# Performance work log

Hardware: AMD Instinct MI355X
Metric: run time of the kernel (lower is better)

## Reference

```python
import jax, jax.numpy as jnp
import numpy as np
from jax import lax

B, CIN, COUT, H, W = 16, 64, 64, 128, 128

def _conv(x, w, b):
    # NCHW conv, 3x3, stride 1, SAME padding (matches nn.Conv2d(k=3,s=1,p=1))
    y = lax.conv_general_dilated(x, w, (1, 1), 'SAME',
                                 dimension_numbers=('NCHW', 'OIHW', 'NCHW'))
    return y + b[None, :, None, None]

def setup_inputs() -> dict:
    key = jax.random.key(0)
    k1, k2, k3, k4, k5 = jax.random.split(key, 5)
    x = jax.random.normal(k1, (B, CIN, H, W), dtype=jnp.float32)
    w_pre = jax.random.normal(k2, (COUT * 4, CIN, 3, 3), dtype=jnp.float32) * 0.05
    b_pre = jax.random.normal(k3, (COUT * 4,), dtype=jnp.float32) * 0.05
    w_post = jax.random.normal(k4, (COUT, COUT, 3, 3), dtype=jnp.float32) * 0.05
    b_post = jax.random.normal(k5, (COUT,), dtype=jnp.float32) * 0.05
    return {'x': x, 'w_pre': w_pre, 'b_pre': b_pre, 'w_post': w_post, 'b_post': b_post}

def reference(x, w_pre, b_pre, w_post, b_post):
    t = _conv(x, w_pre, b_pre)                      # [B, 4C, H, W]
    C = t.shape[1] // 4
    ll = t[:, :C]
    lh = t[:, C:2 * C]      # passed as cV ('ad') to pywt.idwt2
    hl = t[:, 2 * C:3 * C]  # passed as cH ('da')
    hh = t[:, 3 * C:]       # cD ('dd')
    # original detaches coeffs before pywt.idwt2 (grad cut); replicate exactly
    ll, lh, hl, hh = (lax.stop_gradient(v) for v in (ll, lh, hl, hh))
    # orthonormal Haar inverse DWT (pywt 'haar' convention):
    ee = 0.5 * (ll + lh + hl + hh)  # x[2i,   2j]
    eo = 0.5 * (ll - lh + hl - hh)  # x[2i,   2j+1]
    oe = 0.5 * (ll + lh - hl - hh)  # x[2i+1, 2j]
    oo = 0.5 * (ll - lh - hl + hh)  # x[2i+1, 2j+1]
    b, c, h, w = ll.shape
    up = jnp.stack([ee, eo, oe, oo], axis=-1).reshape(b, c, h, w, 2, 2)
    up = up.transpose(0, 1, 2, 4, 3, 5).reshape(b, c, 2 * h, 2 * w)  # pixel shuffle
    return _conv(up, w_post, b_post)
```

## Files before the change

### kernel.cpp

```cpp
#include <hip/hip_runtime.h>
#include <hip/hip_bf16.h>

typedef __attribute__((ext_vector_type(8))) short bf16x8;
typedef __attribute__((ext_vector_type(4))) float f32x4;
typedef __attribute__((ext_vector_type(4))) int   i32x4;

static __device__ __forceinline__ short f2bf(float f) {
  __hip_bfloat16 h = __float2bfloat16(f);
  return *reinterpret_cast<short*>(&h);
}

__global__ __launch_bounds__(256) void prep_xb_k(const float* __restrict__ x,
                                                 short* __restrict__ xb) {
  int u = blockIdx.x * 256 + threadIdx.x;
  int c8  = u & 7;
  int pxl = u >> 3;
  int b   = pxl >> 14;
  int yx  = pxl & 16383;
  bf16x8 r;
  #pragma unroll
  for (int j = 0; j < 8; ++j)
    r[j] = f2bf(x[(b * 64 + c8 * 8 + j) * 16384 + yx]);
  *reinterpret_cast<bf16x8*>(xb + pxl * 64 + c8 * 8) = r;
}

__global__ __launch_bounds__(256) void prep_w1_k(const float* __restrict__ w,
                                                 short* __restrict__ wb) {
  int u = blockIdx.x * 256 + threadIdx.x;
  int o = u / 576;
  int k = u - o * 576;
  int tap = k >> 6, ci = k & 63;
  wb[u] = f2bf(w[(o * 64 + ci) * 9 + tap]);
}

__global__ __launch_bounds__(256) void prep_w2_k(const float* __restrict__ w,
                                                 short* __restrict__ wb) {
  int u = blockIdx.x * 256 + threadIdx.x;
  int o = u / 576;
  int k = u - o * 576;
  int tap = k >> 6, ci = k & 63;
  wb[u] = f2bf(w[(o * 64 + ci) * 9 + tap]);
}

__global__ __launch_bounds__(256) void conv1_k(
    const short* __restrict__ xb,
    const short* __restrict__ wb1,
    const float* __restrict__ b_pre,
    short* __restrict__ up)
{
  __shared__ __align__(16) char sm[25344];
  const int tid = threadIdx.x;
  const int x0  = (blockIdx.x & 1) << 6;
  const int y   = blockIdx.y;
  const int b   = blockIdx.z;

  for (int u = tid; u < 1584; u += 256) {
    int row = u / 528;
    int rem = u - row * 528;
    int px  = rem >> 3;
    int g   = rem & 7;
    int gy  = y + row - 1;
    int gx  = x0 - 1 + px;
    i32x4 v = {0, 0, 0, 0};
    if ((unsigned)gy < 128u && (unsigned)gx < 128u)
      v = *reinterpret_cast<const i32x4*>(xb + (((b << 7) + gy) << 7) * 64 + gx * 64 + g * 8);
    *reinterpret_cast<i32x4*>(sm + ((row * 66 + px) << 7) + ((g * 16) ^ ((px & 7) << 4))) = v;
  }
  __syncthreads();

  const int lane = tid & 63;
  const int wid  = tid >> 6;
  const int ln15 = lane & 15;
  const int g4   = lane >> 4;
  const int cw   = wid << 4;

  f32x4 acc[4][4];
  #pragma unroll
  for (int m = 0; m < 4; ++m)
    #pragma unroll
    for (int v = 0; v < 4; ++v)
      acc[m][v] = (f32x4){0.f, 0.f, 0.f, 0.f};

  for (int tap = 0; tap < 9; ++tap) {
    const int kh = tap / 3;
    const int kw = tap - kh * 3;
    bf16x8 bf[2][4];
    #pragma unroll
    for (int ks = 0; ks < 2; ++ks)
      #pragma unroll
      for (int v = 0; v < 4; ++v)
        bf[ks][v] = *reinterpret_cast<const bf16x8*>(
            wb1 + (v * 64 + cw + ln15) * 576 + tap * 64 + ks * 32 + g4 * 8);
    #pragma unroll
    for (int ks = 0; ks < 2; ++ks) {
      bf16x8 af[4];
      #pragma unroll
      for (int m = 0; m < 4; ++m) {
        int px = m * 16 + ln15 + kw;
        af[m] = *reinterpret_cast<const bf16x8*>(
            sm + ((kh * 66 + px) << 7) + ((ks * 64 + g4 * 16) ^ ((px & 7) << 4)));
      }
      #pragma unroll
      for (int m = 0; m < 4; ++m)
        #pragma unroll
        for (int v = 0; v < 4; ++v)
          acc[m][v] = __builtin_amdgcn_mfma_f32_16x16x32_bf16(af[m], bf[ks][v], acc[m][v], 0, 0, 0);
    }
  }

  const int c = cw + ln15;
  const float bb0 = b_pre[c], bb1 = b_pre[64 + c], bb2 = b_pre[128 + c], bb3 = b_pre[192 + c];
  #pragma unroll
  for (int m = 0; m < 4; ++m) {
    #pragma unroll
    for (int j = 0; j < 4; ++j) {
      int X   = m * 16 + g4 * 4 + j;
      int gxo = (x0 + X) << 1;
      float a0 = acc[m][0][j] + bb0;
      float a1 = acc[m][1][j] + bb1;
      float a2 = acc[m][2][j] + bb2;
      float a3 = acc[m][3][j] + bb3;
      float ee = 0.5f * (a0 + a1 + a2 + a3);
      float eo = 0.5f * (a0 - a1 + a2 - a3);
      float oe = 0.5f * (a0 + a1 - a2 - a3);
      float oo = 0.5f * (a0 - a1 - a2 + a3);
      int base0 = ((((b << 8) + (y << 1)) << 8) + gxo) * 64 + c;
      int base1 = base0 + 256 * 64;
      up[base0]      = f2bf(ee);
      up[base0 + 64] = f2bf(eo);
      up[base1]      = f2bf(oe);
      up[base1 + 64] = f2bf(oo);
    }
  }
}

__global__ __launch_bounds__(256) void conv2_k(
    const short* __restrict__ up,
    const short* __restrict__ wb2,
    const float* __restrict__ b_post,
    float* __restrict__ out)
{
  __shared__ __align__(16) char sm[49920];
  const int tid = threadIdx.x;
  const int x0  = (blockIdx.x & 1) << 7;
  const int y   = blockIdx.y;
  const int b   = blockIdx.z;

  for (int u = tid; u < 3120; u += 256) {
    int row = u / 1040;
    int rem = u - row * 1040;
    int px  = rem >> 3;
    int g   = rem & 7;
    int gy  = y + row - 1;
    int gx  = x0 - 1 + px;
    i32x4 v = {0, 0, 0, 0};
    if ((unsigned)gy < 256u && (unsigned)gx < 256u)
      v = *reinterpret_cast<const i32x4*>(up + ((((b << 8) + gy) << 8) + gx) * 64 + g * 8);
    *reinterpret_cast<i32x4*>(sm + ((row * 130 + px) << 7) + ((g * 16) ^ ((px & 7) << 4))) = v;
  }
  __syncthreads();

  const int lane = tid & 63;
  const int wid  = tid >> 6;
  const int ln15 = lane & 15;
  const int g4   = lane >> 4;
  const int wm   = wid >> 1;
  const int wn   = wid & 1;

  f32x4 acc[4][2];
  #pragma unroll
  for (int m = 0; m < 4; ++m)
    #pragma unroll
    for (int n = 0; n < 2; ++n)
      acc[m][n] = (f32x4){0.f, 0.f, 0.f, 0.f};

  for (int tap = 0; tap < 9; ++tap) {
    const int kh = tap / 3;
    const int kw = tap - kh * 3;
    bf16x8 bf[2][2];
    #pragma unroll
    for (int ks = 0; ks < 2; ++ks)
      #pragma unroll
      for (int n = 0; n < 2; ++n)
        bf[ks][n] = *reinterpret_cast<const bf16x8*>(
            wb2 + (wn * 32 + n * 16 + ln15) * 576 + tap * 64 + ks * 32 + g4 * 8);
    #pragma unroll
    for (int ks = 0; ks < 2; ++ks) {
      bf16x8 af[4];
      #pragma unroll
      for (int m = 0; m < 4; ++m) {
        int px = wm * 64 + m * 16 + ln15 + kw;
        af[m] = *reinterpret_cast<const bf16x8*>(
            sm + ((kh * 130 + px) << 7) + ((ks * 64 + g4 * 16) ^ ((px & 7) << 4)));
      }
      #pragma unroll
      for (int m = 0; m < 4; ++m)
        #pragma unroll
        for (int n = 0; n < 2; ++n)
          acc[m][n] = __builtin_amdgcn_mfma_f32_16x16x32_bf16(af[m], bf[ks][n], acc[m][n], 0, 0, 0);
    }
  }

  #pragma unroll
  for (int n = 0; n < 2; ++n) {
    int o = wn * 32 + n * 16 + ln15;
    float bias = b_post[o];
    #pragma unroll
    for (int m = 0; m < 4; ++m) {
      int X = x0 + wm * 64 + m * 16 + g4 * 4;
      f32x4 vv = acc[m][n] + bias;
      *reinterpret_cast<f32x4*>(out + ((b * 64 + o) * 256 + y) * 256 + X) = vv;
    }
  }
}

extern "C" void kernel_launch(void* const* d_in, const int* in_sizes, int n_in,
                              void* d_out, int out_size, void* d_ws, size_t ws_size,
                              hipStream_t stream) {
  const float* x      = (const float*)d_in[0];
  const float* w_pre  = (const float*)d_in[1];
  const float* b_pre  = (const float*)d_in[2];
  const float* w_post = (const float*)d_in[3];
  const float* b_post = (const float*)d_in[4];
  float* out = (float*)d_out;

  short* xb = (short*)d_out;

  char* ws = (char*)d_ws;
  short* wb1 = (short*)ws;
  short* wb2 = (short*)(ws + 294912);
  short* up  = (short*)(ws + 294912 + 73728);

  prep_xb_k<<<8192, 256, 0, stream>>>(x, xb);
  prep_w1_k<<<576, 256, 0, stream>>>(w_pre, wb1);
  prep_w2_k<<<144, 256, 0, stream>>>(w_post, wb2);

  dim3 g1(2, 128, 16);
  conv1_k<<<g1, 256, 0, stream>>>(xb, wb1, b_pre, up);

  dim3 g2(2, 256, 16);
  conv2_k<<<g2, 256, 0, stream>>>(up, wb2, b_post, out);
}
```

Measured before the change: 677.9 us.

## Tile both convolutions over four output rows per block to reuse halo

conv1 now handles four output rows per block, loading a 6-row halo strip once and looping over rows, so input reloads for the 3x3 window drop from 3x to 1.5x. conv2 switches to 64-pixel by 4-row tiles where each wave computes all 64 output channels for one row, with the same halo reuse. The cost is more shared memory per block (about 50KB), which lowers occupancy, plus fewer blocks in conv1.

```diff
diff --git a/kernel.cpp b/kernel.cpp
--- a/kernel.cpp
+++ b/kernel.cpp
@@ -48,18 +48,18 @@
     const float* __restrict__ b_pre,
     short* __restrict__ up)
 {
-  __shared__ __align__(16) char sm[25344];
+  __shared__ __align__(16) char sm[50688];
   const int tid = threadIdx.x;
-  const int x0  = (blockIdx.x & 1) << 6;
-  const int y   = blockIdx.y;
+  const int x0  = blockIdx.x << 6;
+  const int y0  = blockIdx.y << 2;
   const int b   = blockIdx.z;
 
-  for (int u = tid; u < 1584; u += 256) {
+  for (int u = tid; u < 3168; u += 256) {
     int row = u / 528;
     int rem = u - row * 528;
     int px  = rem >> 3;
     int g   = rem & 7;
-    int gy  = y + row - 1;
+    int gy  = y0 + row - 1;
     int gx  = x0 - 1 + px;
     i32x4 v = {0, 0, 0, 0};
     if ((unsigned)gy < 128u && (unsigned)gx < 128u)
@@ -73,63 +73,66 @@
   const int ln15 = lane & 15;
   const int g4   = lane >> 4;
   const int cw   = wid << 4;
-
-  f32x4 acc[4][4];
-  #pragma unroll
-  for (int m = 0; m < 4; ++m)
-    #pragma unroll
-    for (int v = 0; v < 4; ++v)
-      acc[m][v] = (f32x4){0.f, 0.f, 0.f, 0.f};
-
-  for (int tap = 0; tap < 9; ++tap) {
-    const int kh = tap / 3;
-    const int kw = tap - kh * 3;
-    bf16x8 bf[2][4];
-    #pragma unroll
-    for (int ks = 0; ks < 2; ++ks)
+  const int c    = cw + ln15;
+  const float bb0 = b_pre[c], bb1 = b_pre[64 + c], bb2 = b_pre[128 + c], bb3 = b_pre[192 + c];
+
+  for (int r = 0; r < 4; ++r) {
+    f32x4 acc[4][4];
+    #pragma unroll
+    for (int m = 0; m < 4; ++m)
       #pragma unroll
       for (int v = 0; v < 4; ++v)
-        bf[ks][v] = *reinterpret_cast<const bf16x8*>(
-            wb1 + (v * 64 + cw + ln15) * 576 + tap * 64 + ks * 32 + g4 * 8);
-    #pragma unroll
-    for (int ks = 0; ks < 2; ++ks) {
-      bf16x8 af[4];
-      #pragma unroll
-      for (int m = 0; m < 4; ++m) {
-        int px = m * 16 + ln15 + kw;
-        af[m] = *reinterpret_cast<const bf16x8*>(
-            sm + ((kh * 66 + px) << 7) + ((ks * 64 + g4 * 16) ^ ((px & 7) << 4)));
+        acc[m][v] = (f32x4){0.f, 0.f, 0.f, 0.f};
+
+    for (int tap = 0; tap < 9; ++tap) {
+      const int kh = tap / 3;
+      const int kw = tap - kh * 3;
+      bf16x8 bf[2][4];
+      #pragma unroll
+      for (int ks = 0; ks < 2; ++ks)
+        #pragma unroll
+        for (int v = 0; v < 4; ++v)
+          bf[ks][v] = *reinterpret_cast<const bf16x8*>(
+              wb1 + (v * 64 + cw + ln15) * 576 + tap * 64 + ks * 32 + g4 * 8);
+      #pragma unroll
+      for (int ks = 0; ks < 2; ++ks) {
+        bf16x8 af[4];
+        #pragma unroll
+        for (int m = 0; m < 4; ++m) {
+          int px = m * 16 + ln15 + kw;
+          af[m] = *reinterpret_cast<const bf16x8*>(
+              sm + (((r + kh) * 66 + px) << 7) + ((ks * 64 + g4 * 16) ^ ((px & 7) << 4)));
+        }
+        #pragma unroll
+        for (int m = 0; m < 4; ++m)
+          #pragma unroll
+          for (int v = 0; v < 4; ++v)
+            acc[m][v] = __builtin_amdgcn_mfma_f32_16x16x32_bf16(af[m], bf[ks][v], acc[m][v], 0, 0, 0);
       }
-      #pragma unroll
-      for (int m = 0; m < 4; ++m)
-        #pragma unroll
-        for (int v = 0; v < 4; ++v)
-          acc[m][v] = __builtin_amdgcn_mfma_f32_16x16x32_bf16(af[m], bf[ks][v], acc[m][v], 0, 0, 0);
-    }
-  }
-
-  const int c = cw + ln15;
-  const float bb0 = b_pre[c], bb1 = b_pre[64 + c], bb2 = b_pre[128 + c], bb3 = b_pre[192 + c];
-  #pragma unroll
-  for (int m = 0; m < 4; ++m) {
-    #pragma unroll
-    for (int j = 0; j < 4; ++j) {
-      int X   = m * 16 + g4 * 4 + j;
-      int gxo = (x0 + X) << 1;
-      float a0 = acc[m][0][j] + bb0;
-      float a1 = acc[m][1][j] + bb1;
-      float a2 = acc[m][2][j] + bb2;
-      float a3 = acc[m][3][j] + bb3;
-      float ee = 0.5f * (a0 + a1 + a2 + a3);
-      float eo = 0.5f * (a0 - a1 + a2 - a3);
-      float oe = 0.5f * (a0 + a1 - a2 - a3);
-      float oo = 0.5f * (a0 - a1 - a2 + a3);
-      int base0 = ((((b << 8) + (y << 1)) << 8) + gxo) * 64 + c;
-      int base1 = base0 + 256 * 64;
-      up[base0]      = f2bf(ee);
-      up[base0 + 64] = f2bf(eo);
-      up[base1]      = f2bf(oe);
-      up[base1 + 64] = f2bf(oo);
+    }
+
+    const int py = (y0 + r) << 1;
+    #pragma unroll
+    for (int m = 0; m < 4; ++m) {
+      #pragma unroll
+      for (int j = 0; j < 4; ++j) {
+        int X   = m * 16 + g4 * 4 + j;
+        int gxo = (x0 + X) << 1;
+        float a0 = acc[m][0][j] + bb0;
+        float a1 = acc[m][1][j] + bb1;
+        float a2 = acc[m][2][j] + bb2;
+        float a3 = acc[m][3][j] + bb3;
+        float ee = 0.5f * (a0 + a1 + a2 + a3);
+        float eo = 0.5f * (a0 - a1 + a2 - a3);
+        float oe = 0.5f * (a0 + a1 - a2 - a3);
+        float oo = 0.5f * (a0 - a1 - a2 + a3);
+        int base0 = ((((b << 8) + py) << 8) + gxo) * 64 + c;
+        int base1 = base0 + 256 * 64;
+        up[base0]      = f2bf(ee);
+        up[base0 + 64] = f2bf(eo);
+        up[base1]      = f2bf(oe);
+        up[base1 + 64] = f2bf(oo);
+      }
     }
   }
 }
@@ -140,23 +143,23 @@
     const float* __restrict__ b_post,
     float* __restrict__ out)
 {
-  __shared__ __align__(16) char sm[49920];
+  __shared__ __align__(16) char sm[50688];
   const int tid = threadIdx.x;
-  const int x0  = (blockIdx.x & 1) << 7;
-  const int y   = blockIdx.y;
+  const int x0  = blockIdx.x << 6;
+  const int y0  = blockIdx.y << 2;
   const int b   = blockIdx.z;
 
-  for (int u = tid; u < 3120; u += 256) {
-    int row = u / 1040;
-    int rem = u - row * 1040;
+  for (int u = tid; u < 3168; u += 256) {
+    int row = u / 528;
+    int rem = u - row * 528;
     int px  = rem >> 3;
     int g   = rem & 7;
-    int gy  = y + row - 1;
+    int gy  = y0 + row - 1;
     int gx  = x0 - 1 + px;
     i32x4 v = {0, 0, 0, 0};
     if ((unsigned)gy < 256u && (unsigned)gx < 256u)
       v = *reinterpret_cast<const i32x4*>(up + ((((b << 8) + gy) << 8) + gx) * 64 + g * 8);
-    *reinterpret_cast<i32x4*>(sm + ((row * 130 + px) << 7) + ((g * 16) ^ ((px & 7) << 4))) = v;
+    *reinterpret_cast<i32x4*>(sm + ((row * 66 + px) << 7) + ((g * 16) ^ ((px & 7) << 4))) = v;
   }
   __syncthreads();
 
@@ -164,50 +167,50 @@
   const int wid  = tid >> 6;
   const int ln15 = lane & 15;
   const int g4   = lane >> 4;
-  const int wm   = wid >> 1;
-  const int wn   = wid & 1;
-
-  f32x4 acc[4][2];
+  const int r    = wid;
+
+  f32x4 acc[4][4];
   #pragma unroll
   for (int m = 0; m < 4; ++m)
     #pragma unroll
-    for (int n = 0; n < 2; ++n)
+    for (int n = 0; n < 4; ++n)
       acc[m][n] = (f32x4){0.f, 0.f, 0.f, 0.f};
 
   for (int tap = 0; tap < 9; ++tap) {
     const int kh = tap / 3;
     const int kw = tap - kh * 3;
-    bf16x8 bf[2][2];
+    bf16x8 bf[2][4];
     #pragma unroll
     for (int ks = 0; ks < 2; ++ks)
       #pragma unroll
-      for (int n = 0; n < 2; ++n)
+      for (int n = 0; n < 4; ++n)
         bf[ks][n] = *reinterpret_cast<const bf16x8*>(
-            wb2 + (wn * 32 + n * 16 + ln15) * 576 + tap * 64 + ks * 32 + g4 * 8);
+            wb2 + (n * 16 + ln15) * 576 + tap * 64 + ks * 32 + g4 * 8);
     #pragma unroll
     for (int ks = 0; ks < 2; ++ks) {
       bf16x8 af[4];
       #pragma unroll
       for (int m = 0; m < 4; ++m) {
-        int px = wm * 64 + m * 16 + ln15 + kw;
+        int px = m * 16 + ln15 + kw;
         af[m] = *reinterpret_cast<const bf16x8*>(
-            sm + ((kh * 130 + px) << 7) + ((ks * 64 + g4 * 16) ^ ((px & 7) << 4)));
+            sm + (((r + kh) * 66 + px) << 7) + ((ks * 64 + g4 * 16) ^ ((px & 7) << 4)));
       }
       #pragma unroll
       for (int m = 0; m < 4; ++m)
         #pragma unroll
-        for (int n = 0; n < 2; ++n)
+        for (int n = 0; n < 4; ++n)
           acc[m][n] = __builtin_amdgcn_mfma_f32_16x16x32_bf16(af[m], bf[ks][n], acc[m][n], 0, 0, 0);
     }
   }
 
+  const int y = y0 + r;
   #pragma unroll
-  for (int n = 0; n < 2; ++n) {
-    int o = wn * 32 + n * 16 + ln15;
+  for (int n = 0; n < 4; ++n) {
+    int o = n * 16 + ln15;
     float bias = b_post[o];
     #pragma unroll
     for (int m = 0; m < 4; ++m) {
-      int X = x0 + wm * 64 + m * 16 + g4 * 4;
+      int X = x0 + m * 16 + g4 * 4;
       f32x4 vv = acc[m][n] + bias;
       *reinterpret_cast<f32x4*>(out + ((b * 64 + o) * 256 + y) * 256 + X) = vv;
     }
@@ -235,9 +238,9 @@
   prep_w1_k<<<576, 256, 0, stream>>>(w_pre, wb1);
   prep_w2_k<<<144, 256, 0, stream>>>(w_post, wb2);
 
-  dim3 g1(2, 128, 16);
+  dim3 g1(2, 32, 16);
   conv1_k<<<g1, 256, 0, stream>>>(xb, wb1, b_pre, up);
 
-  dim3 g2(2, 256, 16);
+  dim3 g2(4, 64, 16);
   conv2_k<<<g2, 256, 0, stream>>>(up, wb2, b_post, out);
 }
```

Result: faster. 606.4 us (-10.6%).
